# Optimization experiments

Measured on AMD Instinct MI355X. Metric: run time of the kernel, lower is better.

Reference implementation:

```python
import jax, jax.numpy as jnp
import numpy as np

NEG_SLOPE = 0.2

def gatv2_layer(x, src, dst, Wl, bl, Wr, br, att, bias, N, concat):
    # Wl/Wr: [F_in, H*C]; att: [H, C]
    H, C = att.shape
    xl = (x @ Wl + bl).reshape(-1, H, C)  # source transform [N,H,C]
    xr = (x @ Wr + br).reshape(-1, H, C)  # target transform [N,H,C]
    e = jax.nn.leaky_relu(xl[src] + xr[dst], NEG_SLOPE)          # [E,H,C]
    logits = jnp.einsum('ehc,hc->eh', e, att)                    # [E,H]
    m = jax.ops.segment_max(logits, dst, num_segments=N)         # [N,H]
    p = jnp.exp(logits - m[dst])
    s = jax.ops.segment_sum(p, dst, num_segments=N)              # [N,H]
    alpha = p / s[dst]                                           # [E,H] softmax per dst
    out = jax.ops.segment_sum(alpha[:, :, None] * xl[src], dst, num_segments=N)  # [N,H,C]
    out = out.reshape(N, H * C) if concat else out.mean(axis=1)
    return out + bias


def setup_inputs() -> dict:
    key = jax.random.key(0)
    N, E, F_in = 50000, 500000, 58
    ks = jax.random.split(key, 16)
    s = 0.1
    inp = {
        'x': jax.random.normal(ks[0], (N, F_in), jnp.float32),
        'edge_index': jax.random.randint(ks[1], (2, E), 0, N, jnp.int64),
        'Wl1': jax.random.normal(ks[2], (F_in, 256), jnp.float32) * s,
        'bl1': jnp.zeros((256,), jnp.float32),
        'Wr1': jax.random.normal(ks[3], (F_in, 256), jnp.float32) * s,
        'br1': jnp.zeros((256,), jnp.float32),
        'att1': jax.random.normal(ks[4], (4, 64), jnp.float32) * s,
        'bias1': jnp.zeros((256,), jnp.float32),
        'Wl2': jax.random.normal(ks[5], (256, 256), jnp.float32) * s,
        'bl2': jnp.zeros((256,), jnp.float32),
        'Wr2': jax.random.normal(ks[6], (256, 256), jnp.float32) * s,
        'br2': jnp.zeros((256,), jnp.float32),
        'att2': jax.random.normal(ks[7], (4, 64), jnp.float32) * s,
        'bias2': jnp.zeros((256,), jnp.float32),
        'Wl3': jax.random.normal(ks[8], (256, 6), jnp.float32) * s,
        'bl3': jnp.zeros((6,), jnp.float32),
        'Wr3': jax.random.normal(ks[9], (256, 6), jnp.float32) * s,
        'br3': jnp.zeros((6,), jnp.float32),
        'att3': jax.random.normal(ks[10], (6, 1), jnp.float32) * s,
        'bias3': jnp.zeros((1,), jnp.float32),
    }
    return inp


def reference(x, edge_index, Wl1, bl1, Wr1, br1, att1, bias1,
              Wl2, bl2, Wr2, br2, att2, bias2,
              Wl3, bl3, Wr3, br3, att3, bias3):
    N = x.shape[0]
    loop = jnp.arange(N, dtype=edge_index.dtype)
    src = jnp.concatenate([edge_index[0], loop])  # self-loops (PyG default)
    dst = jnp.concatenate([edge_index[1], loop])
    h = jax.nn.elu(gatv2_layer(x, src, dst, Wl1, bl1, Wr1, br1, att1, bias1, N, True))
    h = jax.nn.elu(gatv2_layer(h, src, dst, Wl2, bl2, Wr2, br2, att2, bias2, N, True))
    out = gatv2_layer(h, src, dst, Wl3, bl3, Wr3, br3, att3, bias3, N, False)
    return out  # [N, 1]
```

## Files before the change

### kernel.cpp

```cpp
#include <hip/hip_runtime.h>
#include <math.h>

#define NEG_SLOPE 0.2f
#define LOG2E 1.4426950408889634f

typedef __attribute__((ext_vector_type(2))) _Float16 h2;
typedef __attribute__((ext_vector_type(4))) _Float16 h4;
typedef __attribute__((ext_vector_type(8))) _Float16 f16x8;
typedef __attribute__((ext_vector_type(4))) float f32x4;

typedef const __attribute__((address_space(1))) unsigned int* gu32p;
typedef __attribute__((address_space(3))) unsigned int* lu32p;

#define GLD16(g, l) __builtin_amdgcn_global_load_lds((gu32p)(g), (lu32p)(l), 16, 0, 0)

template<int CTRL>
__device__ __forceinline__ float dpp_add_f32(float x) {
    int y = __builtin_amdgcn_update_dpp(0, __float_as_int(x), CTRL, 0xF, 0xF, true);
    return x + __int_as_float(y);
}
__device__ __forceinline__ float rowsum16(float x) {
    x = dpp_add_f32<0xB1>(x);
    x = dpp_add_f32<0x4E>(x);
    x = dpp_add_f32<0x124>(x);
    x = dpp_add_f32<0x128>(x);
    return x;
}


__global__ __launch_bounds__(256) void k_scan_block(const int* __restrict__ cnt,
                                                    int* __restrict__ out,
                                                    int* __restrict__ bsums, int n) {
    __shared__ int tmp[256];
    int t = threadIdx.x;
    int i = blockIdx.x * 256 + t;
    int v = (i < n) ? cnt[i] : 0;
    tmp[t] = v;
    __syncthreads();
    for (int d = 1; d < 256; d <<= 1) {
        int add = (t >= d) ? tmp[t - d] : 0;
        __syncthreads();
        tmp[t] += add;
        __syncthreads();
    }
    if (i < n) out[i] = tmp[t] - v;
    if (t == 255) bsums[blockIdx.x] = tmp[t];
}

__global__ __launch_bounds__(256) void k_scan_bsums(int* bsums, int nb) {
    __shared__ int tmp[256];
    int t = threadIdx.x;
    int v = (t < nb) ? bsums[t] : 0;
    tmp[t] = v;
    __syncthreads();
    for (int d = 1; d < 256; d <<= 1) {
        int add = (t >= d) ? tmp[t - d] : 0;
        __syncthreads();
        tmp[t] += add;
        __syncthreads();
    }
    if (t < nb) bsums[t] = tmp[t] - v;
}

__global__ __launch_bounds__(256) void k_scan_add(int* __restrict__ out,
                                                  const int* __restrict__ bsums,
                                                  int* __restrict__ cursor,
                                                  int n, int total) {
    int i = blockIdx.x * 256 + threadIdx.x;
    if (i < n) {
        int v = out[i] + bsums[blockIdx.x];
        out[i] = v;
        cursor[i] = v;
    }
    if (i == 0) out[n] = total;
}

__global__ __launch_bounds__(256) void k_scatter(const int* __restrict__ ei, int E, int Et,
                                                 int* __restrict__ cursor,
                                                 int* __restrict__ src_sorted) {
    int e = blockIdx.x * 256 + threadIdx.x;
    if (e < Et) {
        int s, d;
        if (e < E) { s = ei[e]; d = ei[E + e]; } else { s = d = e - E; }
        int pos = atomicAdd(&cursor[d], 1);
        src_sorted[pos] = s;
    }
}


__global__ __launch_bounds__(256) void k_prep(
        const int* __restrict__ ei, int E, int Et, int* __restrict__ cnt,
        const float* __restrict__ x, _Float16* __restrict__ xb, int N, int F,
        const float* __restrict__ Wl1, const float* __restrict__ Wr1,
        const float* __restrict__ Wl2, const float* __restrict__ Wr2,
        const float* __restrict__ Wl3, const float* __restrict__ Wr3,
        _Float16* __restrict__ wtl1, _Float16* __restrict__ wtr1,
        _Float16* __restrict__ wtl2, _Float16* __restrict__ wtr2,
        _Float16* __restrict__ w3t, int gEt, int gX) {
    const int b = blockIdx.x;
    if (b < gEt) {
        int e = b * 256 + threadIdx.x;
        if (e < Et) {
            int d = (e < E) ? ei[E + e] : (e - E);
            atomicAdd(&cnt[d], 1);
        }
    } else if (b < gEt + gX) {
        int i = (b - gEt) * 256 + threadIdx.x;
        if (i < (N << 6)) {
            int n = i >> 6, k = i & 63;
            xb[i] = (_Float16)(k < F ? x[n * F + k] : 0.0f);
        }
    } else {
        int i = (b - gEt - gX) * 256 + threadIdx.x;
        if (i < 32768) {
            const float* W = (i < 16384) ? Wl1 : Wr1;
            _Float16* O = (i < 16384) ? wtl1 : wtr1;
            int loc = i & 16383;
            int n = loc >> 6, k = loc & 63;
            O[loc] = (_Float16)(k < F ? W[k * 256 + n] : 0.0f);
        } else if (i < 163840) {
            int seg = i - 32768;
            const float* W = (seg < 65536) ? Wl2 : Wr2;
            _Float16* O = (seg < 65536) ? wtl2 : wtr2;
            int loc = seg & 65535;
            int n = loc >> 8, k = loc & 255;
            O[loc] = (_Float16)W[k * 256 + n];
        } else if (i < 167936) {
            int loc = i - 163840;
            int j = loc >> 8, k = loc & 255;
            float v = (j < 6) ? Wl3[k * 6 + j] : ((j < 12) ? Wr3[k * 6 + (j - 6)] : 0.0f);
            w3t[loc] = (_Float16)v;
        }
    }
}


__global__ __launch_bounds__(256) void k_gemm_pair_mfma(
        const _Float16* __restrict__ A, int M, int Kp,
        const _Float16* __restrict__ Btl, const _Float16* __restrict__ Btr,
        const float* __restrict__ bl, const float* __restrict__ br,
        _Float16* __restrict__ Cl, _Float16* __restrict__ Cr) {
    __shared__ _Float16 As[128 * 32];
    __shared__ _Float16 Bs[128 * 32];
    const int wv = threadIdx.x >> 6, lane = threadIdx.x & 63;
    const int wr = wv >> 1, wc = wv & 1;
    const int l15 = lane & 15, l4 = lane >> 4;
    const int row0 = blockIdx.x * 128;
    const int mat  = blockIdx.y >> 1;
    const int col0 = (blockIdx.y & 1) * 128;
    const _Float16* Bt = mat ? Btr : Btl;
    const float* bias  = mat ? br  : bl;
    _Float16* C        = mat ? Cr  : Cl;

    const int rl = lane >> 2;
    const int kq = (lane & 3) * 8;
    const _Float16* ga0 = A + (size_t)min(row0 + wv * 32 + rl,      M - 1) * Kp + kq;
    const _Float16* ga1 = A + (size_t)min(row0 + wv * 32 + 16 + rl, M - 1) * Kp + kq;
    const _Float16* gb0 = Bt + (size_t)(col0 + wv * 32 + rl) * Kp + kq;
    const _Float16* gb1 = Bt + (size_t)(col0 + wv * 32 + 16 + rl) * Kp + kq;
    _Float16* la0 = &As[(wv * 32) * 32];
    _Float16* la1 = &As[(wv * 32 + 16) * 32];
    _Float16* lb0 = &Bs[(wv * 32) * 32];
    _Float16* lb1 = &Bs[(wv * 32 + 16) * 32];

    f32x4 acc[4][4];
    #pragma unroll
    for (int a = 0; a < 4; a++)
        #pragma unroll
        for (int b = 0; b < 4; b++)
            acc[a][b] = (f32x4){0.f, 0.f, 0.f, 0.f};

    for (int k0 = 0; k0 < Kp; k0 += 32) {
        GLD16(ga0 + k0, la0);
        GLD16(ga1 + k0, la1);
        GLD16(gb0 + k0, lb0);
        GLD16(gb1 + k0, lb1);
        __syncthreads();
        f16x8 wf[4], xf[4];
        #pragma unroll
        for (int ct = 0; ct < 4; ct++)
            wf[ct] = *(const f16x8*)&Bs[(wc * 64 + ct * 16 + l15) * 32 + l4 * 8];
        #pragma unroll
        for (int nt = 0; nt < 4; nt++)
            xf[nt] = *(const f16x8*)&As[(wr * 64 + nt * 16 + l15) * 32 + l4 * 8];
        #pragma unroll
        for (int ct = 0; ct < 4; ct++)
            #pragma unroll
            for (int nt = 0; nt < 4; nt++)
                acc[ct][nt] = __builtin_amdgcn_mfma_f32_16x16x32_f16(
                    wf[ct], xf[nt], acc[ct][nt], 0, 0, 0);
        __syncthreads();
    }

    float4 bv[4];
    #pragma unroll
    for (int ct = 0; ct < 4; ct++)
        bv[ct] = *(const float4*)&bias[col0 + wc * 64 + ct * 16 + l4 * 4];
    #pragma unroll
    for (int nt = 0; nt < 4; nt++) {
        int node = row0 + wr * 64 + nt * 16 + l15;
        if (node < M) {
            #pragma unroll
            for (int ct = 0; ct < 4; ct++) {
                h4 hv = {(_Float16)(acc[ct][nt][0] + bv[ct].x),
                         (_Float16)(acc[ct][nt][1] + bv[ct].y),
                         (_Float16)(acc[ct][nt][2] + bv[ct].z),
                         (_Float16)(acc[ct][nt][3] + bv[ct].w)};
                *(h4*)&C[(size_t)node * 256 + col0 + wc * 64 + ct * 16 + l4 * 4] = hv;
            }
        }
    }
}


__global__ __launch_bounds__(256) void k_gemm3_mfma(
        const _Float16* __restrict__ h,
        const _Float16* __restrict__ W3t,
        const float* __restrict__ bl, const float* __restrict__ br,
        _Float16* __restrict__ l3, int N) {
    const int wave = threadIdx.x >> 6, lane = threadIdx.x & 63;
    const int l15 = lane & 15, l4 = lane >> 4;
    const int row0 = blockIdx.x * 64 + wave * 16;
    if (row0 >= N) return;

    f16x8 bfr[8];
    #pragma unroll
    for (int ks = 0; ks < 8; ks++)
        bfr[ks] = *(const f16x8*)&W3t[l15 * 256 + ks * 32 + l4 * 8];

    const int arow = min(row0 + l15, N - 1);
    const size_t abase = (size_t)arow * 256;
    f32x4 acc = (f32x4){0.f, 0.f, 0.f, 0.f};
    #pragma unroll
    for (int ks = 0; ks < 8; ks++) {
        f16x8 af = *(const f16x8*)&h[abase + ks * 32 + l4 * 8];
        acc = __builtin_amdgcn_mfma_f32_16x16x32_f16(af, bfr[ks], acc, 0, 0, 0);
    }
    const float bv = (l15 < 6) ? bl[l15] : ((l15 < 12) ? br[l15 - 6] : 0.0f);
    #pragma unroll
    for (int r = 0; r < 4; r++) {
        int gr = row0 + l4 * 4 + r;
        if (gr < N && l15 < 12)
            l3[(size_t)gr * 16 + l15] = (_Float16)(acc[r] + bv);
    }
}


__global__ __launch_bounds__(256) void k_agg256(const _Float16* __restrict__ xl,
                                                const _Float16* __restrict__ xr,
                                                const int* __restrict__ row_ptr,
                                                const int* __restrict__ src_sorted,
                                                const float* __restrict__ att,
                                                const float* __restrict__ bias,
                                                _Float16* __restrict__ h_out, int N) {
    const int wave = threadIdx.x >> 6;
    const int lane = threadIdx.x & 63;
    const int n = __builtin_amdgcn_readfirstlane(blockIdx.x * 4 + wave);
    if (n >= N) return;
    const int ci = lane * 4;
    const h4 xr4 = *(const h4*)&xr[(size_t)n * 256 + ci];
    const float4 at4 = *(const float4*)&att[ci];
    const h2 ata = {(_Float16)(at4.x * LOG2E), (_Float16)(at4.y * LOG2E)};
    const h2 atb = {(_Float16)(at4.z * LOG2E), (_Float16)(at4.w * LOG2E)};
    float a0 = 0.f, a1 = 0.f, a2 = 0.f, a3 = 0.f;
    float m = -INFINITY, s = 0.0f;
    const int beg = row_ptr[n], end = row_ptr[n + 1];

    int j = beg;
    h4 v[8], vn[8];
    #pragma unroll
    for (int e = 0; e < 8; e++) {
        int idx = j + e;
        idx = idx < end ? idx : end - 1;
        int sv = src_sorted[idx];
        v[e] = *(const h4*)&xl[(size_t)sv * 256 + ci];
    }
    while (true) {
        const int jn = j + 8;
        const bool hasN = (jn < end);
        if (hasN) {
            #pragma unroll
            for (int e = 0; e < 8; e++) {
                int idx = jn + e;
                idx = idx < end ? idx : end - 1;
                int sv = src_sorted[idx];
                vn[e] = *(const h4*)&xl[(size_t)sv * 256 + ci];
            }
        }
        float lg[8];
        #pragma unroll
        for (int e = 0; e < 8; e++) {
            h4 t = v[e] + xr4;
            h4 lk = __builtin_elementwise_max(t, t * (_Float16)NEG_SLOPE);
            h2 lo = __builtin_shufflevector(lk, lk, 0, 1);
            h2 hi = __builtin_shufflevector(lk, lk, 2, 3);
            lg[e] = __builtin_amdgcn_fdot2(lo, ata,
                        __builtin_amdgcn_fdot2(hi, atb, 0.0f, false), false);
        }
        #pragma unroll
        for (int e = 0; e < 8; e++) lg[e] = rowsum16(lg[e]);
        #pragma unroll
        for (int e = 0; e < 8; e++)
            if (j + e >= end) lg[e] = -INFINITY;
        float bm = fmaxf(fmaxf(fmaxf(lg[0], lg[1]), fmaxf(lg[2], lg[3])),
                         fmaxf(fmaxf(lg[4], lg[5]), fmaxf(lg[6], lg[7])));
        float nm = fmaxf(m, bm);
        float sc = __builtin_amdgcn_exp2f(m - nm);
        a0 *= sc; a1 *= sc; a2 *= sc; a3 *= sc;
        float ps = 0.f;
        #pragma unroll
        for (int e = 0; e < 8; e++) {
            float p = __builtin_amdgcn_exp2f(lg[e] - nm);
            ps += p;
            a0 = fmaf(p, (float)v[e].x, a0);
            a1 = fmaf(p, (float)v[e].y, a1);
            a2 = fmaf(p, (float)v[e].z, a2);
            a3 = fmaf(p, (float)v[e].w, a3);
        }
        s = s * sc + ps;
        m = nm;
        if (!hasN) break;
        #pragma unroll
        for (int e = 0; e < 8; e++) v[e] = vn[e];
        j = jn;
    }
    const float inv = 1.0f / s;
    const float4 bv = *(const float4*)&bias[ci];
    float o0 = a0 * inv + bv.x;
    float o1 = a1 * inv + bv.y;
    float o2 = a2 * inv + bv.z;
    float o3 = a3 * inv + bv.w;
    o0 = o0 > 0.f ? o0 : (__expf(o0) - 1.f);
    o1 = o1 > 0.f ? o1 : (__expf(o1) - 1.f);
    o2 = o2 > 0.f ? o2 : (__expf(o2) - 1.f);
    o3 = o3 > 0.f ? o3 : (__expf(o3) - 1.f);
    h4 hv = {(_Float16)o0, (_Float16)o1, (_Float16)o2, (_Float16)o3};
    *(h4*)&h_out[(size_t)n * 256 + ci] = hv;
}


__global__ __launch_bounds__(256) void k_agg3(const _Float16* __restrict__ l3,
                                              const int* __restrict__ row_ptr,
                                              const int* __restrict__ src_sorted,
                                              const float* __restrict__ att3,
                                              const float* __restrict__ bias3,
                                              float* __restrict__ out, int N) {
    int n = blockIdx.x * 256 + threadIdx.x;
    if (n >= N) return;
    const h4* pn = (const h4*)&l3[(size_t)n * 16];
    h4 q1 = pn[1], q2 = pn[2];
    float xrv[6];
    xrv[0] = (float)q1.z; xrv[1] = (float)q1.w;
    xrv[2] = (float)q2.x; xrv[3] = (float)q2.y;
    xrv[4] = (float)q2.z; xrv[5] = (float)q2.w;
    float attv[6], m[6], s[6], acc[6];
    #pragma unroll
    for (int k = 0; k < 6; k++) {
        attv[k] = att3[k] * LOG2E;
        m[k] = -INFINITY; s[k] = 0.0f; acc[k] = 0.0f;
    }
    const int beg = row_ptr[n], end = row_ptr[n + 1];
    for (int j = beg; j < end; j += 8) {
        f16x8 u[8];
        #pragma unroll
        for (int e = 0; e < 8; e++) {
            int idx = j + e;
            idx = idx < end ? idx : end - 1;
            int sv = src_sorted[idx];
            u[e] = *(const f16x8*)&l3[(size_t)sv * 16];
        }
        #pragma unroll
        for (int e = 0; e < 8; e++) {
            const bool valid = (j + e) < end;
            float xlv[6];
            #pragma unroll
            for (int k = 0; k < 6; k++) xlv[k] = (float)u[e][k];
            #pragma unroll
            for (int k = 0; k < 6; k++) {
                float tt = xlv[k] + xrv[k];
                float lr = fmaxf(tt, NEG_SLOPE * tt);
                float logit = valid ? (attv[k] * lr) : -INFINITY;
                float nm = fmaxf(m[k], logit);
                float sc = __builtin_amdgcn_exp2f(m[k] - nm);
                float p  = __builtin_amdgcn_exp2f(logit - nm);
                acc[k] = acc[k] * sc + p * xlv[k];
                s[k]   = s[k] * sc + p;
                m[k]   = nm;
            }
        }
    }
    float o = 0.0f;
    #pragma unroll
    for (int k = 0; k < 6; k++) o += acc[k] / s[k];
    out[n] = o * (1.0f / 6.0f) + bias3[0];
}


extern "C" void kernel_launch(void* const* d_in, const int* in_sizes, int n_in,
                              void* d_out, int out_size, void* d_ws, size_t ws_size,
                              hipStream_t stream) {
    const float* x    = (const float*)d_in[0];
    const int*   ei   = (const int*)  d_in[1];
    const float* Wl1  = (const float*)d_in[2];
    const float* bl1  = (const float*)d_in[3];
    const float* Wr1  = (const float*)d_in[4];
    const float* br1  = (const float*)d_in[5];
    const float* att1 = (const float*)d_in[6];
    const float* bias1= (const float*)d_in[7];
    const float* Wl2  = (const float*)d_in[8];
    const float* bl2  = (const float*)d_in[9];
    const float* Wr2  = (const float*)d_in[10];
    const float* br2  = (const float*)d_in[11];
    const float* att2 = (const float*)d_in[12];
    const float* bias2= (const float*)d_in[13];
    const float* Wl3  = (const float*)d_in[14];
    const float* bl3  = (const float*)d_in[15];
    const float* Wr3  = (const float*)d_in[16];
    const float* br3  = (const float*)d_in[17];
    const float* att3 = (const float*)d_in[18];
    const float* bias3= (const float*)d_in[19];

    const int F  = in_sizes[2] / 256;
    const int N  = in_sizes[0] / F;
    const int E  = in_sizes[1] / 2;
    const int Et = E + N;

    char* ws = (char*)d_ws;
    size_t off = 0;
    auto carve = [&](size_t bytes) -> char* {
        char* p = ws + off;
        off = (off + bytes + 255) & ~(size_t)255;
        return p;
    };
    _Float16* xb   = (_Float16*)carve((size_t)N * 64 * 2);
    _Float16* xlb  = (_Float16*)carve((size_t)N * 256 * 2);
    _Float16* xrb  = (_Float16*)carve((size_t)N * 256 * 2);
    _Float16* hb   = (_Float16*)carve((size_t)N * 256 * 2);
    _Float16* wtl1 = (_Float16*)carve(256 * 64 * 2);
    _Float16* wtr1 = (_Float16*)carve(256 * 64 * 2);
    _Float16* wtl2 = (_Float16*)carve(256 * 256 * 2);
    _Float16* wtr2 = (_Float16*)carve(256 * 256 * 2);
    _Float16* w3t  = (_Float16*)carve(16 * 256 * 2);
    _Float16* l3   = (_Float16*)carve((size_t)N * 16 * 2);
    int* cnt        = (int*)carve((size_t)N * 4);
    int* row_ptr    = (int*)carve((size_t)(N + 1) * 4);
    int* cursor     = (int*)carve((size_t)N * 4);
    int* src_sorted = (int*)carve((size_t)Et * 4);
    int* bsums      = (int*)carve(1024 * 4);

    const int gN  = (N + 255) / 256;
    const int gEt = (Et + 255) / 256;
    const int gX  = ((N << 6) + 255) / 256;
    const int gW  = (N + 3) / 4;

    hipMemsetAsync(cnt, 0, (size_t)N * 4, stream);
    k_prep<<<gEt + gX + 656, 256, 0, stream>>>(ei, E, Et, cnt, x, xb, N, F,
                                               Wl1, Wr1, Wl2, Wr2, Wl3, Wr3,
                                               wtl1, wtr1, wtl2, wtr2, w3t, gEt, gX);

    k_scan_block<<<gN, 256, 0, stream>>>(cnt, row_ptr, bsums, N);
    k_scan_bsums<<<1, 256, 0, stream>>>(bsums, gN);
    k_scan_add<<<gN, 256, 0, stream>>>(row_ptr, bsums, cursor, N, Et);
    k_scatter<<<gEt, 256, 0, stream>>>(ei, E, Et, cursor, src_sorted);

    dim3 gemm_grid((N + 127) / 128, 4);

    k_gemm_pair_mfma<<<gemm_grid, 256, 0, stream>>>(xb, N, 64, wtl1, wtr1, bl1, br1, xlb, xrb);
    k_agg256<<<gW, 256, 0, stream>>>(xlb, xrb, row_ptr, src_sorted, att1, bias1, hb, N);

    k_gemm_pair_mfma<<<gemm_grid, 256, 0, stream>>>(hb, N, 256, wtl2, wtr2, bl2, br2, xlb, xrb);
    k_agg256<<<gW, 256, 0, stream>>>(xlb, xrb, row_ptr, src_sorted, att2, bias2, hb, N);

    k_gemm3_mfma<<<(N + 63) / 64, 256, 0, stream>>>(hb, w3t, bl3, br3, l3, N);
    k_agg3<<<(N + 255) / 256, 256, 0, stream>>>(l3, row_ptr, src_sorted, att3, bias3,
                                                (float*)d_out, N);
}
```

Baseline: 335.6 us.

## Split edges across wave halves in aggregation, widen GEMM tile, fuse scan kernels

The aggregation kernel now has each lane own 8 channels, and the two half-waves process alternate edges, each with its own online softmax. The two halves are merged with a cross-lane shuffle at the end, which halves the per-edge reduction width and issues 16-byte gathers. Tail edges are handled separately with masking. The pair GEMM moves to 512-thread blocks that cover all 256 output columns, so each A tile is loaded once per matrix. The block-sum scan is folded into the scan-add kernel, removing one launch. The cost is more registers and extra control-flow complexity for the tail handling.

```diff
diff --git a/kernel.cpp b/kernel.cpp
--- a/kernel.cpp
+++ b/kernel.cpp
@@ -3,6 +3,7 @@
 
 #define NEG_SLOPE 0.2f
 #define LOG2E 1.4426950408889634f
+#define MNEG 1.0e30f
 
 typedef __attribute__((ext_vector_type(2))) _Float16 h2;
 typedef __attribute__((ext_vector_type(4))) _Float16 h4;
@@ -19,11 +20,10 @@
     int y = __builtin_amdgcn_update_dpp(0, __float_as_int(x), CTRL, 0xF, 0xF, true);
     return x + __int_as_float(y);
 }
-__device__ __forceinline__ float rowsum16(float x) {
+__device__ __forceinline__ float rowsum8_bcast(float x) {
     x = dpp_add_f32<0xB1>(x);
     x = dpp_add_f32<0x4E>(x);
-    x = dpp_add_f32<0x124>(x);
-    x = dpp_add_f32<0x128>(x);
+    x = dpp_add_f32<0x141>(x);
     return x;
 }
 
@@ -47,7 +47,10 @@
     if (t == 255) bsums[blockIdx.x] = tmp[t];
 }
 
-__global__ __launch_bounds__(256) void k_scan_bsums(int* bsums, int nb) {
+__global__ __launch_bounds__(256) void k_scan_add(int* __restrict__ out,
+                                                  const int* __restrict__ bsums,
+                                                  int* __restrict__ cursor,
+                                                  int n, int total, int nb) {
     __shared__ int tmp[256];
     int t = threadIdx.x;
     int v = (t < nb) ? bsums[t] : 0;
@@ -59,18 +62,12 @@
         tmp[t] += add;
         __syncthreads();
     }
-    if (t < nb) bsums[t] = tmp[t] - v;
-}
-
-__global__ __launch_bounds__(256) void k_scan_add(int* __restrict__ out,
-                                                  const int* __restrict__ bsums,
-                                                  int* __restrict__ cursor,
-                                                  int n, int total) {
-    int i = blockIdx.x * 256 + threadIdx.x;
+    int boff = tmp[blockIdx.x] - bsums[blockIdx.x];
+    int i = blockIdx.x * 256 + t;
     if (i < n) {
-        int v = out[i] + bsums[blockIdx.x];
-        out[i] = v;
-        cursor[i] = v;
+        int vv = out[i] + boff;
+        out[i] = vv;
+        cursor[i] = vv;
     }
     if (i == 0) out[n] = total;
 }
@@ -135,33 +132,31 @@
 }
 
 
-__global__ __launch_bounds__(256) void k_gemm_pair_mfma(
+__global__ __launch_bounds__(512) void k_gemm_pair_mfma(
         const _Float16* __restrict__ A, int M, int Kp,
         const _Float16* __restrict__ Btl, const _Float16* __restrict__ Btr,
         const float* __restrict__ bl, const float* __restrict__ br,
         _Float16* __restrict__ Cl, _Float16* __restrict__ Cr) {
     __shared__ _Float16 As[128 * 32];
-    __shared__ _Float16 Bs[128 * 32];
-    const int wv = threadIdx.x >> 6, lane = threadIdx.x & 63;
-    const int wr = wv >> 1, wc = wv & 1;
+    __shared__ _Float16 Bs[256 * 32];
+    const int tid = threadIdx.x;
+    const int wv = tid >> 6, lane = tid & 63;
+    const int wr = wv >> 2, wc = wv & 3;
     const int l15 = lane & 15, l4 = lane >> 4;
     const int row0 = blockIdx.x * 128;
-    const int mat  = blockIdx.y >> 1;
-    const int col0 = (blockIdx.y & 1) * 128;
+    const int mat  = blockIdx.y;
     const _Float16* Bt = mat ? Btr : Btl;
     const float* bias  = mat ? br  : bl;
     _Float16* C        = mat ? Cr  : Cl;
 
-    const int rl = lane >> 2;
-    const int kq = (lane & 3) * 8;
-    const _Float16* ga0 = A + (size_t)min(row0 + wv * 32 + rl,      M - 1) * Kp + kq;
-    const _Float16* ga1 = A + (size_t)min(row0 + wv * 32 + 16 + rl, M - 1) * Kp + kq;
-    const _Float16* gb0 = Bt + (size_t)(col0 + wv * 32 + rl) * Kp + kq;
-    const _Float16* gb1 = Bt + (size_t)(col0 + wv * 32 + 16 + rl) * Kp + kq;
-    _Float16* la0 = &As[(wv * 32) * 32];
-    _Float16* la1 = &As[(wv * 32 + 16) * 32];
-    _Float16* lb0 = &Bs[(wv * 32) * 32];
-    _Float16* lb1 = &Bs[(wv * 32 + 16) * 32];
+    const int sr = tid >> 2;
+    const int sk = (tid & 3) * 8;
+    const _Float16* gA  = A  + (size_t)min(row0 + sr, M - 1) * Kp + sk;
+    const _Float16* gB0 = Bt + (size_t)sr * Kp + sk;
+    const _Float16* gB1 = Bt + (size_t)(sr + 128) * Kp + sk;
+    _Float16* lA  = &As[(wv * 16) * 32];
+    _Float16* lB0 = &Bs[(wv * 16) * 32];
+    _Float16* lB1 = &Bs[(wv * 16 + 128) * 32];
 
     f32x4 acc[4][4];
     #pragma unroll
@@ -171,10 +166,9 @@
             acc[a][b] = (f32x4){0.f, 0.f, 0.f, 0.f};
 
     for (int k0 = 0; k0 < Kp; k0 += 32) {
-        GLD16(ga0 + k0, la0);
-        GLD16(ga1 + k0, la1);
-        GLD16(gb0 + k0, lb0);
-        GLD16(gb1 + k0, lb1);
+        GLD16(gA + k0, lA);
+        GLD16(gB0 + k0, lB0);
+        GLD16(gB1 + k0, lB1);
         __syncthreads();
         f16x8 wf[4], xf[4];
         #pragma unroll
@@ -195,7 +189,7 @@
     float4 bv[4];
     #pragma unroll
     for (int ct = 0; ct < 4; ct++)
-        bv[ct] = *(const float4*)&bias[col0 + wc * 64 + ct * 16 + l4 * 4];
+        bv[ct] = *(const float4*)&bias[wc * 64 + ct * 16 + l4 * 4];
     #pragma unroll
     for (int nt = 0; nt < 4; nt++) {
         int node = row0 + wr * 64 + nt * 16 + l15;
@@ -206,7 +200,7 @@
                          (_Float16)(acc[ct][nt][1] + bv[ct].y),
                          (_Float16)(acc[ct][nt][2] + bv[ct].z),
                          (_Float16)(acc[ct][nt][3] + bv[ct].w)};
-                *(h4*)&C[(size_t)node * 256 + col0 + wc * 64 + ct * 16 + l4 * 4] = hv;
+                *(h4*)&C[(size_t)node * 256 + wc * 64 + ct * 16 + l4 * 4] = hv;
             }
         }
     }
@@ -245,6 +239,67 @@
     }
 }
 
+
+__device__ __forceinline__ float edge_logit(const f16x8 v, const f16x8 xr8,
+        const h2 at0, const h2 at1, const h2 at2, const h2 at3) {
+    f16x8 t = v + xr8;
+    f16x8 lk = __builtin_elementwise_max(t, t * (_Float16)NEG_SLOPE);
+    h2 c0 = __builtin_shufflevector(lk, lk, 0, 1);
+    h2 c1 = __builtin_shufflevector(lk, lk, 2, 3);
+    h2 c2 = __builtin_shufflevector(lk, lk, 4, 5);
+    h2 c3 = __builtin_shufflevector(lk, lk, 6, 7);
+    float d = __builtin_amdgcn_fdot2(c0, at0,
+              __builtin_amdgcn_fdot2(c1, at1,
+              __builtin_amdgcn_fdot2(c2, at2,
+              __builtin_amdgcn_fdot2(c3, at3, 0.0f, false), false), false), false);
+    return rowsum8_bcast(d);
+}
+
+__device__ __forceinline__ void batch8(const f16x8 v0, const f16x8 v1,
+                                       const f16x8 v2, const f16x8 v3,
+                                       int pcn, int invp, bool hi,
+                                       const f16x8 xr8,
+                                       const h2 at0, const h2 at1,
+                                       const h2 at2, const h2 at3,
+                                       float* a, float& m, float& s) {
+    float lg0 = -INFINITY, lg1 = -INFINITY, lg2 = -INFINITY, lg3 = -INFINITY;
+    if (pcn > 0) lg0 = edge_logit(v0, xr8, at0, at1, at2, at3);
+    if (pcn > 1) lg1 = edge_logit(v1, xr8, at0, at1, at2, at3);
+    if (pcn > 2) lg2 = edge_logit(v2, xr8, at0, at1, at2, at3);
+    if (pcn > 3) lg3 = edge_logit(v3, xr8, at0, at1, at2, at3);
+    if (invp == 0) lg0 = hi ? -INFINITY : lg0;
+    if (invp == 1) lg1 = hi ? -INFINITY : lg1;
+    if (invp == 2) lg2 = hi ? -INFINITY : lg2;
+    if (invp == 3) lg3 = hi ? -INFINITY : lg3;
+    float bm = fmaxf(fmaxf(lg0, lg1), fmaxf(lg2, lg3));
+    float nm = fmaxf(m, bm);
+    float sc = __builtin_amdgcn_exp2f(m - nm);
+    #pragma unroll
+    for (int c = 0; c < 8; c++) a[c] *= sc;
+    float ps = 0.f;
+    if (pcn > 0) {
+        float pe = __builtin_amdgcn_exp2f(lg0 - nm); ps += pe;
+        #pragma unroll
+        for (int c = 0; c < 8; c++) a[c] = fmaf(pe, (float)v0[c], a[c]);
+    }
+    if (pcn > 1) {
+        float pe = __builtin_amdgcn_exp2f(lg1 - nm); ps += pe;
+        #pragma unroll
+        for (int c = 0; c < 8; c++) a[c] = fmaf(pe, (float)v1[c], a[c]);
+    }
+    if (pcn > 2) {
+        float pe = __builtin_amdgcn_exp2f(lg2 - nm); ps += pe;
+        #pragma unroll
+        for (int c = 0; c < 8; c++) a[c] = fmaf(pe, (float)v2[c], a[c]);
+    }
+    if (pcn > 3) {
+        float pe = __builtin_amdgcn_exp2f(lg3 - nm); ps += pe;
+        #pragma unroll
+        for (int c = 0; c < 8; c++) a[c] = fmaf(pe, (float)v3[c], a[c]);
+    }
+    s = s * sc + ps;
+    m = nm;
+}
 
 __global__ __launch_bounds__(256) void k_agg256(const _Float16* __restrict__ xl,
                                                 const _Float16* __restrict__ xr,
@@ -257,85 +312,111 @@
     const int lane = threadIdx.x & 63;
     const int n = __builtin_amdgcn_readfirstlane(blockIdx.x * 4 + wave);
     if (n >= N) return;
-    const int ci = lane * 4;
-    const h4 xr4 = *(const h4*)&xr[(size_t)n * 256 + ci];
-    const float4 at4 = *(const float4*)&att[ci];
-    const h2 ata = {(_Float16)(at4.x * LOG2E), (_Float16)(at4.y * LOG2E)};
-    const h2 atb = {(_Float16)(at4.z * LOG2E), (_Float16)(at4.w * LOG2E)};
-    float a0 = 0.f, a1 = 0.f, a2 = 0.f, a3 = 0.f;
-    float m = -INFINITY, s = 0.0f;
+    const bool hi = lane >= 32;
+    const int ci = (lane & 7) * 8 + ((lane >> 3) & 3) * 64;
+
+    const f16x8 xr8 = *(const f16x8*)&xr[(size_t)n * 256 + ci];
+    const float4 af0 = *(const float4*)&att[ci];
+    const float4 af1 = *(const float4*)&att[ci + 4];
+    const h2 at0 = {(_Float16)(af0.x * LOG2E), (_Float16)(af0.y * LOG2E)};
+    const h2 at1 = {(_Float16)(af0.z * LOG2E), (_Float16)(af0.w * LOG2E)};
+    const h2 at2 = {(_Float16)(af1.x * LOG2E), (_Float16)(af1.y * LOG2E)};
+    const h2 at3 = {(_Float16)(af1.z * LOG2E), (_Float16)(af1.w * LOG2E)};
+
+    float a[8];
+    #pragma unroll
+    for (int c = 0; c < 8; c++) a[c] = 0.f;
+    float m = -MNEG, s = 0.0f;
+
     const int beg = row_ptr[n], end = row_ptr[n + 1];
+    const int deg = end - beg;
+    const int rem = deg & 7;
+    const int tb  = end - rem;
+    const int pc  = (rem + 1) >> 1;
+    const int invp = (rem & 1) ? (pc - 1) : -1;
+
+    f16x8 vt0, vt1, vt2, vt3;
+    if (pc > 0) { int ia = src_sorted[tb];
+                  int ib = src_sorted[min(tb + 1, end - 1)];
+                  int sv = hi ? ib : ia;
+                  vt0 = *(const f16x8*)&xl[(size_t)sv * 256 + ci]; }
+    if (pc > 1) { int ia = src_sorted[tb + 2];
+                  int ib = src_sorted[min(tb + 3, end - 1)];
+                  int sv = hi ? ib : ia;
+                  vt1 = *(const f16x8*)&xl[(size_t)sv * 256 + ci]; }
+    if (pc > 2) { int ia = src_sorted[tb + 4];
+                  int ib = src_sorted[min(tb + 5, end - 1)];
+                  int sv = hi ? ib : ia;
+                  vt2 = *(const f16x8*)&xl[(size_t)sv * 256 + ci]; }
+    if (pc > 3) { int ia = src_sorted[tb + 6];
+                  int ib = src_sorted[min(tb + 7, end - 1)];
+                  int sv = hi ? ib : ia;
+                  vt3 = *(const f16x8*)&xl[(size_t)sv * 256 + ci]; }
 
     int j = beg;
-    h4 v[8], vn[8];
-    #pragma unroll
-    for (int e = 0; e < 8; e++) {
-        int idx = j + e;
-        idx = idx < end ? idx : end - 1;
-        int sv = src_sorted[idx];
-        v[e] = *(const h4*)&xl[(size_t)sv * 256 + ci];
-    }
-    while (true) {
+    f16x8 v0, v1, v2, v3, w0, w1, w2, w3;
+    bool has = (j + 8 <= tb);
+    if (has) {
+        int i0 = src_sorted[j],     i1 = src_sorted[j + 1];
+        int i2 = src_sorted[j + 2], i3 = src_sorted[j + 3];
+        int i4 = src_sorted[j + 4], i5 = src_sorted[j + 5];
+        int i6 = src_sorted[j + 6], i7 = src_sorted[j + 7];
+        int s0 = hi ? i1 : i0, s1 = hi ? i3 : i2, s2 = hi ? i5 : i4, s3 = hi ? i7 : i6;
+        v0 = *(const f16x8*)&xl[(size_t)s0 * 256 + ci];
+        v1 = *(const f16x8*)&xl[(size_t)s1 * 256 + ci];
+        v2 = *(const f16x8*)&xl[(size_t)s2 * 256 + ci];
+        v3 = *(const f16x8*)&xl[(size_t)s3 * 256 + ci];
+    }
+    while (has) {
         const int jn = j + 8;
-        const bool hasN = (jn < end);
+        const bool hasN = (jn + 8 <= tb);
         if (hasN) {
-            #pragma unroll
-            for (int e = 0; e < 8; e++) {
-                int idx = jn + e;
-                idx = idx < end ? idx : end - 1;
-                int sv = src_sorted[idx];
-                vn[e] = *(const h4*)&xl[(size_t)sv * 256 + ci];
-            }
-        }
-        float lg[8];
-        #pragma unroll
-        for (int e = 0; e < 8; e++) {
-            h4 t = v[e] + xr4;
-            h4 lk = __builtin_elementwise_max(t, t * (_Float16)NEG_SLOPE);
-            h2 lo = __builtin_shufflevector(lk, lk, 0, 1);
-            h2 hi = __builtin_shufflevector(lk, lk, 2, 3);
-            lg[e] = __builtin_amdgcn_fdot2(lo, ata,
-                        __builtin_amdgcn_fdot2(hi, atb, 0.0f, false), false);
-        }
-        #pragma unroll
-        for (int e = 0; e < 8; e++) lg[e] = rowsum16(lg[e]);
-        #pragma unroll
-        for (int e = 0; e < 8; e++)
-            if (j + e >= end) lg[e] = -INFINITY;
-        float bm = fmaxf(fmaxf(fmaxf(lg[0], lg[1]), fmaxf(lg[2], lg[3])),
-                         fmaxf(fmaxf(lg[4], lg[5]), fmaxf(lg[6], lg[7])));
-        float nm = fmaxf(m, bm);
-        float sc = __builtin_amdgcn_exp2f(m - nm);
-        a0 *= sc; a1 *= sc; a2 *= sc; a3 *= sc;
-        float ps = 0.f;
-        #pragma unroll
-        for (int e = 0; e < 8; e++) {
-            float p = __builtin_amdgcn_exp2f(lg[e] - nm);
-            ps += p;
-            a0 = fmaf(p, (float)v[e].x, a0);
-            a1 = fmaf(p, (float)v[e].y, a1);
-            a2 = fmaf(p, (float)v[e].z, a2);
-            a3 = fmaf(p, (float)v[e].w, a3);
-        }
-        s = s * sc + ps;
-        m = nm;
-        if (!hasN) break;
-        #pragma unroll
-        for (int e = 0; e < 8; e++) v[e] = vn[e];
+            int i0 = src_sorted[jn],     i1 = src_sorted[jn + 1];
+            int i2 = src_sorted[jn + 2], i3 = src_sorted[jn + 3];
+            int i4 = src_sorted[jn + 4], i5 = src_sorted[jn + 5];
+            int i6 = src_sorted[jn + 6], i7 = src_sorted[jn + 7];
+            int s0 = hi ? i1 : i0, s1 = hi ? i3 : i2, s2 = hi ? i5 : i4, s3 = hi ? i7 : i6;
+            w0 = *(const f16x8*)&xl[(size_t)s0 * 256 + ci];
+            w1 = *(const f16x8*)&xl[(size_t)s1 * 256 + ci];
+            w2 = *(const f16x8*)&xl[(size_t)s2 * 256 + ci];
+            w3 = *(const f16x8*)&xl[(size_t)s3 * 256 + ci];
+        }
+        batch8(v0, v1, v2, v3, 4, -1, hi, xr8, at0, at1, at2, at3, a, m, s);
+        if (hasN) { v0 = w0; v1 = w1; v2 = w2; v3 = w3; }
         j = jn;
-    }
-    const float inv = 1.0f / s;
-    const float4 bv = *(const float4*)&bias[ci];
-    float o0 = a0 * inv + bv.x;
-    float o1 = a1 * inv + bv.y;
-    float o2 = a2 * inv + bv.z;
-    float o3 = a3 * inv + bv.w;
-    o0 = o0 > 0.f ? o0 : (__expf(o0) - 1.f);
-    o1 = o1 > 0.f ? o1 : (__expf(o1) - 1.f);
-    o2 = o2 > 0.f ? o2 : (__expf(o2) - 1.f);
-    o3 = o3 > 0.f ? o3 : (__expf(o3) - 1.f);
-    h4 hv = {(_Float16)o0, (_Float16)o1, (_Float16)o2, (_Float16)o3};
-    *(h4*)&h_out[(size_t)n * 256 + ci] = hv;
+        has = hasN;
+    }
+
+    if (pc)
+        batch8(vt0, vt1, vt2, vt3, pc, invp, hi, xr8, at0, at1, at2, at3, a, m, s);
+
+    float om = __shfl_xor(m, 32);
+    float os = __shfl_xor(s, 32);
+    float qa[8];
+    #pragma unroll
+    for (int c = 0; c < 8; c++) qa[c] = __shfl_xor(a[c], 32);
+
+    float nm = fmaxf(m, om);
+    float e0 = __builtin_amdgcn_exp2f(m - nm);
+    float e1 = __builtin_amdgcn_exp2f(om - nm);
+    float stot = s * e0 + os * e1;
+    float inv = 1.0f / stot;
+
+    const float4 b0 = *(const float4*)&bias[ci];
+    const float4 b1 = *(const float4*)&bias[ci + 4];
+    float bb[8] = {b0.x, b0.y, b0.z, b0.w, b1.x, b1.y, b1.z, b1.w};
+
+    _Float16 hv[8];
+    #pragma unroll
+    for (int c = 0; c < 8; c++) {
+        float o = (a[c] * e0 + qa[c] * e1) * inv + bb[c];
+        o = o > 0.f ? o : (__expf(o) - 1.f);
+        hv[c] = (_Float16)o;
+    }
+    if (!hi) {
+        f16x8 hv8 = {hv[0], hv[1], hv[2], hv[3], hv[4], hv[5], hv[6], hv[7]};
+        *(f16x8*)&h_out[(size_t)n * 256 + ci] = hv8;
+    }
 }
 
 
@@ -459,16 +540,15 @@
                                                wtl1, wtr1, wtl2, wtr2, w3t, gEt, gX);
 
     k_scan_block<<<gN, 256, 0, stream>>>(cnt, row_ptr, bsums, N);
-    k_scan_bsums<<<1, 256, 0, stream>>>(bsums, gN);
-    k_scan_add<<<gN, 256, 0, stream>>>(row_ptr, bsums, cursor, N, Et);
+    k_scan_add<<<gN, 256, 0, stream>>>(row_ptr, bsums, cursor, N, Et, gN);
     k_scatter<<<gEt, 256, 0, stream>>>(ei, E, Et, cursor, src_sorted);
 
-    dim3 gemm_grid((N + 127) / 128, 4);
-
-    k_gemm_pair_mfma<<<gemm_grid, 256, 0, stream>>>(xb, N, 64, wtl1, wtr1, bl1, br1, xlb, xrb);
+    dim3 gemm_grid((N + 127) / 128, 2);
+
+    k_gemm_pair_mfma<<<gemm_grid, 512, 0, stream>>>(xb, N, 64, wtl1, wtr1, bl1, br1, xlb, xrb);
     k_agg256<<<gW, 256, 0, stream>>>(xlb, xrb, row_ptr, src_sorted, att1, bias1, hb, N);
 
-    k_gemm_pair_mfma<<<gemm_grid, 256, 0, stream>>>(hb, N, 256, wtl2, wtr2, bl2, br2, xlb, xrb);
+    k_gemm_pair_mfma<<<gemm_grid, 512, 0, stream>>>(hb, N, 256, wtl2, wtr2, bl2, br2, xlb, xrb);
     k_agg256<<<gW, 256, 0, stream>>>(xlb, xrb, row_ptr, src_sorted, att2, bias2, hb, N);
 
     k_gemm3_mfma<<<(N + 63) / 64, 256, 0, stream>>>(hb, w3t, bl3, br3, l3, N);
```

New measurement: 327.7 us. 1.02x faster.
